# Kernel optimization log

Hardware: AMD Instinct MI355X
Metric: run time of the kernel (lower is better)

## Reference

```python
import jax, jax.numpy as jnp
import numpy as np

N_ITERS = 21
TEMPERATURE = 0.01


def setup_inputs() -> dict:
    key = jax.random.key(0)
    input_tensor = jax.random.normal(key, (512, 256, 256), dtype=jnp.float32)
    return {"input_tensor": input_tensor}


def reference(input_tensor) -> jnp.ndarray:
    # log_alpha: [B, n, n]
    n = input_tensor.shape[1]
    log_alpha = input_tensor.reshape(-1, n, n) / TEMPERATURE

    def body(i, la):
        # row normalization (sum over dim 2), then column normalization (sum over dim 1)
        la = la - jax.nn.logsumexp(la, axis=2, keepdims=True)
        la = la - jax.nn.logsumexp(la, axis=1, keepdims=True)
        return la

    log_alpha = jax.lax.fori_loop(0, N_ITERS, body, log_alpha)
    return jnp.exp(log_alpha)
```

## Files before the change

### kernel.cpp

```cpp
#include <hip/hip_runtime.h>

typedef __attribute__((ext_vector_type(2))) float f32x2;

#define N 256
#define BLK 1024
#define N_ITERS 21

template <int CTRL>
__device__ __forceinline__ float dppmov(float v) {
  return __int_as_float(__builtin_amdgcn_update_dpp(
      0, __float_as_int(v), CTRL, 0xF, 0xF, true));
}
__device__ __forceinline__ float swz_xor16(float v) {
  return __int_as_float(
      __builtin_amdgcn_ds_swizzle(__float_as_int(v), 0x401F));
}
__device__ __forceinline__ float rsum32(float v) {
  v += dppmov<0x121>(v);
  v += dppmov<0x122>(v);
  v += dppmov<0x124>(v);
  v += dppmov<0x128>(v);
  v += swz_xor16(v);
  return v;
}
__device__ __forceinline__ float rmax32(float v) {
  v = fmaxf(v, dppmov<0x121>(v));
  v = fmaxf(v, dppmov<0x122>(v));
  v = fmaxf(v, dppmov<0x124>(v));
  v = fmaxf(v, dppmov<0x128>(v));
  v = fmaxf(v, swz_xor16(v));
  return v;
}
__device__ __forceinline__ f32x2 pkmax(f32x2 a, f32x2 b) {
  f32x2 r;
  r.x = fmaxf(a.x, b.x);
  r.y = fmaxf(a.y, b.y);
  return r;
}

__global__ __launch_bounds__(BLK, 2)
void sinkhorn_kernel(const float* __restrict__ x, float* __restrict__ out) {
  __shared__ float lds_part[32 * N];
  __shared__ float lds_v[N];

  const int tid = threadIdx.x;
  const int cg = tid & 31;
  const int rg = tid >> 5;
  const int r0 = rg * 8;
  const long mat = blockIdx.x;
  const float SCALE = 144.2695040888963407f;

  const int cr = tid >> 2;
  const int q = tid & 3;
  const int cg_r = cr & 31;
  const int k_r = cr >> 5;
  const int red_base = k_r * 32;
  const int vslot = k_r * 32 + cg_r;

  const float4* __restrict__ src4 =
      reinterpret_cast<const float4*>(x + mat * (long)(N * N));
  f32x2 p[8][4];
  #pragma unroll
  for (int r = 0; r < 8; ++r) {
    float4 a = src4[(r0 + r) * 64 + cg * 2];
    float4 b = src4[(r0 + r) * 64 + cg * 2 + 1];
    f32x2 t;
    t.x = a.x; t.y = a.y; p[r][0] = t * SCALE;
    t.x = a.z; t.y = a.w; p[r][1] = t * SCALE;
    t.x = b.x; t.y = b.y; p[r][2] = t * SCALE;
    t.x = b.z; t.y = b.w; p[r][3] = t * SCALE;
  }

  f32x2 Vr[4];

  #pragma unroll
  for (int r = 0; r < 8; ++r) {
    f32x2 m2 = pkmax(pkmax(p[r][0], p[r][1]), pkmax(p[r][2], p[r][3]));
    float m = rmax32(fmaxf(m2.x, m2.y));
    float s = 0.f;
    #pragma unroll
    for (int j = 0; j < 4; ++j) {
      s += __builtin_amdgcn_exp2f(p[r][j].x - m);
      s += __builtin_amdgcn_exp2f(p[r][j].y - m);
    }
    s = rsum32(s);
    float L = m + __builtin_amdgcn_logf(s);
    #pragma unroll
    for (int j = 0; j < 4; ++j) p[r][j] -= L;
  }
  {
    f32x2 cm[4];
    #pragma unroll
    for (int j = 0; j < 4; ++j) cm[j] = p[0][j];
    #pragma unroll
    for (int r = 1; r < 8; ++r)
      #pragma unroll
      for (int j = 0; j < 4; ++j) cm[j] = pkmax(cm[j], p[r][j]);
    const int wslot = (cg + rg) & 31;
    #pragma unroll
    for (int j = 0; j < 4; ++j) {
      lds_part[rg * N + (2 * j) * 32 + wslot] = cm[j].x;
      lds_part[rg * N + (2 * j + 1) * 32 + wslot] = cm[j].y;
    }
    __syncthreads();
    float M = -3.0e38f;
    #pragma unroll
    for (int jj = 0; jj < 8; ++jj) {
      int h = q * 8 + jj;
      M = fmaxf(M, lds_part[h * N + red_base + ((cg_r + h) & 31)]);
    }
    M = fmaxf(M, dppmov<0xB1>(M));
    M = fmaxf(M, dppmov<0x4E>(M));
    if (q == 0) lds_v[vslot] = M;
    __syncthreads();
    f32x2 Mk[4];
    #pragma unroll
    for (int j = 0; j < 4; ++j) {
      Mk[j].x = lds_v[(2 * j) * 32 + cg];
      Mk[j].y = lds_v[(2 * j + 1) * 32 + cg];
    }
    f32x2 ps[4];
    #pragma unroll
    for (int j = 0; j < 4; ++j) { ps[j].x = 0.f; ps[j].y = 0.f; }
    #pragma unroll
    for (int r = 0; r < 8; ++r) {
      #pragma unroll
      for (int j = 0; j < 4; ++j) {
        f32x2 v;
        v.x = __builtin_amdgcn_exp2f(p[r][j].x - Mk[j].x);
        v.y = __builtin_amdgcn_exp2f(p[r][j].y - Mk[j].y);
        p[r][j] = v;
        ps[j] += v;
      }
    }
    #pragma unroll
    for (int j = 0; j < 4; ++j) {
      lds_part[rg * N + (2 * j) * 32 + wslot] = ps[j].x;
      lds_part[rg * N + (2 * j + 1) * 32 + wslot] = ps[j].y;
    }
    __syncthreads();
    float S = 0.f;
    #pragma unroll
    for (int jj = 0; jj < 8; ++jj) {
      int h = q * 8 + jj;
      S += lds_part[h * N + red_base + ((cg_r + h) & 31)];
    }
    S += dppmov<0xB1>(S);
    S += dppmov<0x4E>(S);
    if (q == 0) lds_v[vslot] = __builtin_amdgcn_rcpf(S);
    __syncthreads();
    #pragma unroll
    for (int j = 0; j < 4; ++j) {
      Vr[j].x = lds_v[(2 * j) * 32 + cg];
      Vr[j].y = lds_v[(2 * j + 1) * 32 + cg];
    }
  }

  for (int it = 1; it < N_ITERS; ++it) {
    f32x2 ps[4];
    #pragma unroll
    for (int j = 0; j < 4; ++j) { ps[j].x = 0.f; ps[j].y = 0.f; }
    #pragma unroll
    for (int r = 0; r < 8; ++r) {
      p[r][0] *= Vr[0]; p[r][1] *= Vr[1];
      p[r][2] *= Vr[2]; p[r][3] *= Vr[3];
      f32x2 t = (p[r][0] + p[r][1]) + (p[r][2] + p[r][3]);
      float g = __builtin_amdgcn_rcpf(rsum32(t.x + t.y));
      p[r][0] *= g; p[r][1] *= g; p[r][2] *= g; p[r][3] *= g;
      ps[0] += p[r][0]; ps[1] += p[r][1];
      ps[2] += p[r][2]; ps[3] += p[r][3];
    }
    const int wslot = (cg + rg) & 31;
    #pragma unroll
    for (int j = 0; j < 4; ++j) {
      lds_part[rg * N + (2 * j) * 32 + wslot] = ps[j].x;
      lds_part[rg * N + (2 * j + 1) * 32 + wslot] = ps[j].y;
    }
    __syncthreads();
    float S = 0.f;
    #pragma unroll
    for (int jj = 0; jj < 8; ++jj) {
      int h = q * 8 + jj;
      S += lds_part[h * N + red_base + ((cg_r + h) & 31)];
    }
    S += dppmov<0xB1>(S);
    S += dppmov<0x4E>(S);
    if (q == 0) lds_v[vslot] = __builtin_amdgcn_rcpf(S);
    __syncthreads();
    #pragma unroll
    for (int j = 0; j < 4; ++j) {
      Vr[j].x = lds_v[(2 * j) * 32 + cg];
      Vr[j].y = lds_v[(2 * j + 1) * 32 + cg];
    }
  }

  float4* __restrict__ dst4 =
      reinterpret_cast<float4*>(out + mat * (long)(N * N));
  #pragma unroll
  for (int r = 0; r < 8; ++r) {
    f32x2 a = p[r][0] * Vr[0];
    f32x2 b = p[r][1] * Vr[1];
    f32x2 c = p[r][2] * Vr[2];
    f32x2 d = p[r][3] * Vr[3];
    dst4[(r0 + r) * 64 + cg * 2] = make_float4(a.x, a.y, b.x, b.y);
    dst4[(r0 + r) * 64 + cg * 2 + 1] = make_float4(c.x, c.y, d.x, d.y);
  }
}

extern "C" void kernel_launch(void* const* d_in, const int* in_sizes, int n_in,
                              void* d_out, int out_size, void* d_ws, size_t ws_size,
                              hipStream_t stream) {
  const float* x = (const float*)d_in[0];
  float* out = (float*)d_out;
  int B = in_sizes[0] / (N * N);
  hipLaunchKernelGGL(sinkhorn_kernel, dim3(B), dim3(BLK), 0, stream, x, out);
}
```

Baseline: 135.8 us.

## Replace LDS tree reductions with triple-buffered LDS atomics and permlane swaps

Column sums and the initial column max are now accumulated with LDS atomicAdd/atomicMin into small triple-rotated buffers rather than written as partials and re-reduced. This cuts each Sinkhorn iteration to one barrier instead of two. The max relies on uint ordering of non-positive floats, which holds because values are log-normalized. Cross-half exchanges use permlane16/32_swap where available instead of ds_swizzle. The cost is 16-way atomic contention per LDS slot.

```diff
diff --git a/kernel.cpp b/kernel.cpp
--- a/kernel.cpp
+++ b/kernel.cpp
@@ -1,35 +1,91 @@
 #include <hip/hip_runtime.h>
 
 typedef __attribute__((ext_vector_type(2))) float f32x2;
+typedef unsigned int uintv2 __attribute__((ext_vector_type(2)));
 
 #define N 256
 #define BLK 1024
-#define N_ITERS 21
+#define SLOTS 290
 
 template <int CTRL>
 __device__ __forceinline__ float dppmov(float v) {
   return __int_as_float(__builtin_amdgcn_update_dpp(
       0, __float_as_int(v), CTRL, 0xF, 0xF, true));
 }
-__device__ __forceinline__ float swz_xor16(float v) {
-  return __int_as_float(
-      __builtin_amdgcn_ds_swizzle(__float_as_int(v), 0x401F));
-}
+
+#if __has_builtin(__builtin_amdgcn_permlane16_swap)
+__device__ __forceinline__ float xor16_add(float x) {
+  uintv2 r = __builtin_amdgcn_permlane16_swap(__float_as_uint(x),
+                                              __float_as_uint(x), false, false);
+  return __uint_as_float(r.x) + __uint_as_float(r.y);
+}
+__device__ __forceinline__ float xor16_max(float x) {
+  uintv2 r = __builtin_amdgcn_permlane16_swap(__float_as_uint(x),
+                                              __float_as_uint(x), false, false);
+  return fmaxf(__uint_as_float(r.x), __uint_as_float(r.y));
+}
+#else
+__device__ __forceinline__ float xor16_add(float x) {
+  return x + __int_as_float(
+                 __builtin_amdgcn_ds_swizzle(__float_as_int(x), 0x401F));
+}
+__device__ __forceinline__ float xor16_max(float x) {
+  return fmaxf(x, __int_as_float(__builtin_amdgcn_ds_swizzle(
+                      __float_as_int(x), 0x401F)));
+}
+#endif
+
+#if __has_builtin(__builtin_amdgcn_permlane32_swap)
+__device__ __forceinline__ void pair32(float x, float& lo, float& hi) {
+  uintv2 r = __builtin_amdgcn_permlane32_swap(__float_as_uint(x),
+                                              __float_as_uint(x), false, false);
+  lo = __uint_as_float(r.x);
+  hi = __uint_as_float(r.y);
+}
+__device__ __forceinline__ float swap32_add(float a, float b) {
+  uintv2 r = __builtin_amdgcn_permlane32_swap(__float_as_uint(a),
+                                              __float_as_uint(b), false, false);
+  return __uint_as_float(r.x) + __uint_as_float(r.y);
+}
+__device__ __forceinline__ float swap32_max(float a, float b) {
+  uintv2 r = __builtin_amdgcn_permlane32_swap(__float_as_uint(a),
+                                              __float_as_uint(b), false, false);
+  return fmaxf(__uint_as_float(r.x), __uint_as_float(r.y));
+}
+#else
+__device__ __forceinline__ void pair32(float x, float& lo, float& hi) {
+  float o = __shfl_xor(x, 32);
+  bool up = (threadIdx.x & 32) != 0;
+  lo = up ? o : x;
+  hi = up ? x : o;
+}
+__device__ __forceinline__ float swap32_add(float a, float b) {
+  bool up = (threadIdx.x & 32) != 0;
+  float mine = up ? b : a;
+  float send = up ? a : b;
+  return mine + __shfl_xor(send, 32);
+}
+__device__ __forceinline__ float swap32_max(float a, float b) {
+  bool up = (threadIdx.x & 32) != 0;
+  float mine = up ? b : a;
+  float send = up ? a : b;
+  return fmaxf(mine, __shfl_xor(send, 32));
+}
+#endif
+
 __device__ __forceinline__ float rsum32(float v) {
   v += dppmov<0x121>(v);
   v += dppmov<0x122>(v);
   v += dppmov<0x124>(v);
   v += dppmov<0x128>(v);
-  v += swz_xor16(v);
-  return v;
+  return xor16_add(v);
 }
 __device__ __forceinline__ float rmax32(float v) {
   v = fmaxf(v, dppmov<0x121>(v));
   v = fmaxf(v, dppmov<0x122>(v));
   v = fmaxf(v, dppmov<0x124>(v));
   v = fmaxf(v, dppmov<0x128>(v));
-  v = fmaxf(v, swz_xor16(v));
-  return v;
+  return xor16_max(v);
 }
 __device__ __forceinline__ f32x2 pkmax(f32x2 a, f32x2 b) {
   f32x2 r;
@@ -38,24 +94,59 @@
   return r;
 }
 
+__device__ __forceinline__ void prob_iter(f32x2 (&p)[8][4], f32x2 (&Vr)[4],
+                                          float* WR, float* ZR, int slot,
+                                          int hi) {
+  f32x2 ps[4];
+  ps[0] = ps[1] = ps[2] = ps[3] = (f32x2){0.f, 0.f};
+  #pragma unroll
+  for (int r = 0; r < 8; ++r) {
+    p[r][0] *= Vr[0]; p[r][1] *= Vr[1];
+    p[r][2] *= Vr[2]; p[r][3] *= Vr[3];
+    f32x2 t2 = (p[r][0] + p[r][1]) + (p[r][2] + p[r][3]);
+    float g = __builtin_amdgcn_rcpf(rsum32(t2.x + t2.y));
+    p[r][0] *= g; p[r][1] *= g; p[r][2] *= g; p[r][3] *= g;
+    ps[0] += p[r][0]; ps[1] += p[r][1];
+    ps[2] += p[r][2]; ps[3] += p[r][3];
+  }
+  const float psf[8] = {ps[0].x, ps[0].y, ps[1].x, ps[1].y,
+                        ps[2].x, ps[2].y, ps[3].x, ps[3].y};
+  #pragma unroll
+  for (int j = 0; j < 4; ++j)
+    atomicAdd(&WR[slot + j], swap32_add(psf[j], psf[j + 4]));
+  #pragma unroll
+  for (int j = 0; j < 4; ++j) ZR[slot + j] = 0.f;
+  __syncthreads();
+  float vf[8];
+  #pragma unroll
+  for (int j = 0; j < 4; ++j) {
+    float s = __builtin_amdgcn_rcpf(WR[slot + j]);
+    pair32(s, vf[j], vf[j + 4]);
+  }
+  Vr[0] = (f32x2){vf[0], vf[1]};
+  Vr[1] = (f32x2){vf[2], vf[3]};
+  Vr[2] = (f32x2){vf[4], vf[5]};
+  Vr[3] = (f32x2){vf[6], vf[7]};
+}
+
 __global__ __launch_bounds__(BLK, 2)
 void sinkhorn_kernel(const float* __restrict__ x, float* __restrict__ out) {
-  __shared__ float lds_part[32 * N];
-  __shared__ float lds_v[N];
+  __shared__ float S0[SLOTS], S1[SLOTS], S2[SLOTS];
 
   const int tid = threadIdx.x;
   const int cg = tid & 31;
   const int rg = tid >> 5;
   const int r0 = rg * 8;
+  const int hi = rg & 1;
+  const int slot = 9 * cg + hi * 4;
   const long mat = blockIdx.x;
   const float SCALE = 144.2695040888963407f;
 
-  const int cr = tid >> 2;
-  const int q = tid & 3;
-  const int cg_r = cr & 31;
-  const int k_r = cr >> 5;
-  const int red_base = k_r * 32;
-  const int vslot = k_r * 32 + cg_r;
+  if (tid < SLOTS) {
+    S0[tid] = 0.f;
+    S1[tid] = 0.f;
+    reinterpret_cast<unsigned*>(S2)[tid] = 0xFFFFFFFFu;
+  }
 
   const float4* __restrict__ src4 =
       reinterpret_cast<const float4*>(x + mat * (long)(N * N));
@@ -71,8 +162,6 @@
     t.x = b.z; t.y = b.w; p[r][3] = t * SCALE;
   }
 
-  f32x2 Vr[4];
-
   #pragma unroll
   for (int r = 0; r < 8; ++r) {
     f32x2 m2 = pkmax(pkmax(p[r][0], p[r][1]), pkmax(p[r][2], p[r][3]));
@@ -88,111 +177,73 @@
     #pragma unroll
     for (int j = 0; j < 4; ++j) p[r][j] -= L;
   }
+  __syncthreads();
+
   {
     f32x2 cm[4];
     #pragma unroll
     for (int j = 0; j < 4; ++j) cm[j] = p[0][j];
     #pragma unroll
-    for (int r = 1; r < 8; ++r)
+    for (int r = 1; r < 8; ++r) {
       #pragma unroll
       for (int j = 0; j < 4; ++j) cm[j] = pkmax(cm[j], p[r][j]);
-    const int wslot = (cg + rg) & 31;
+    }
+    const float cmf[8] = {cm[0].x, cm[0].y, cm[1].x, cm[1].y,
+                          cm[2].x, cm[2].y, cm[3].x, cm[3].y};
+    unsigned* S2u = reinterpret_cast<unsigned*>(S2);
+    #pragma unroll
+    for (int j = 0; j < 4; ++j)
+      atomicMin(&S2u[slot + j],
+                __float_as_uint(swap32_max(cmf[j], cmf[j + 4])));
+    __syncthreads();
+    float Mf[8];
     #pragma unroll
     for (int j = 0; j < 4; ++j) {
-      lds_part[rg * N + (2 * j) * 32 + wslot] = cm[j].x;
-      lds_part[rg * N + (2 * j + 1) * 32 + wslot] = cm[j].y;
-    }
-    __syncthreads();
-    float M = -3.0e38f;
-    #pragma unroll
-    for (int jj = 0; jj < 8; ++jj) {
-      int h = q * 8 + jj;
-      M = fmaxf(M, lds_part[h * N + red_base + ((cg_r + h) & 31)]);
-    }
-    M = fmaxf(M, dppmov<0xB1>(M));
-    M = fmaxf(M, dppmov<0x4E>(M));
-    if (q == 0) lds_v[vslot] = M;
-    __syncthreads();
-    f32x2 Mk[4];
-    #pragma unroll
-    for (int j = 0; j < 4; ++j) {
-      Mk[j].x = lds_v[(2 * j) * 32 + cg];
-      Mk[j].y = lds_v[(2 * j + 1) * 32 + cg];
+      float xx = __uint_as_float(S2u[slot + j]);
+      pair32(xx, Mf[j], Mf[j + 4]);
     }
     f32x2 ps[4];
-    #pragma unroll
-    for (int j = 0; j < 4; ++j) { ps[j].x = 0.f; ps[j].y = 0.f; }
+    ps[0] = ps[1] = ps[2] = ps[3] = (f32x2){0.f, 0.f};
     #pragma unroll
     for (int r = 0; r < 8; ++r) {
       #pragma unroll
-      for (int j = 0; j < 4; ++j) {
+      for (int k = 0; k < 4; ++k) {
         f32x2 v;
-        v.x = __builtin_amdgcn_exp2f(p[r][j].x - Mk[j].x);
-        v.y = __builtin_amdgcn_exp2f(p[r][j].y - Mk[j].y);
-        p[r][j] = v;
-        ps[j] += v;
+        v.x = __builtin_amdgcn_exp2f(p[r][k].x - Mf[2 * k]);
+        v.y = __builtin_amdgcn_exp2f(p[r][k].y - Mf[2 * k + 1]);
+        p[r][k] = v;
+        ps[k] += v;
       }
     }
+    const float psf[8] = {ps[0].x, ps[0].y, ps[1].x, ps[1].y,
+                          ps[2].x, ps[2].y, ps[3].x, ps[3].y};
+    #pragma unroll
+    for (int j = 0; j < 4; ++j)
+      atomicAdd(&S0[slot + j], swap32_add(psf[j], psf[j + 4]));
+    __syncthreads();
+  }
+  f32x2 Vr[4];
+  {
+    float vf[8];
     #pragma unroll
     for (int j = 0; j < 4; ++j) {
-      lds_part[rg * N + (2 * j) * 32 + wslot] = ps[j].x;
-      lds_part[rg * N + (2 * j + 1) * 32 + wslot] = ps[j].y;
-    }
-    __syncthreads();
-    float S = 0.f;
-    #pragma unroll
-    for (int jj = 0; jj < 8; ++jj) {
-      int h = q * 8 + jj;
-      S += lds_part[h * N + red_base + ((cg_r + h) & 31)];
-    }
-    S += dppmov<0xB1>(S);
-    S += dppmov<0x4E>(S);
-    if (q == 0) lds_v[vslot] = __builtin_amdgcn_rcpf(S);
-    __syncthreads();
-    #pragma unroll
-    for (int j = 0; j < 4; ++j) {
-      Vr[j].x = lds_v[(2 * j) * 32 + cg];
-      Vr[j].y = lds_v[(2 * j + 1) * 32 + cg];
-    }
-  }
-
-  for (int it = 1; it < N_ITERS; ++it) {
-    f32x2 ps[4];
-    #pragma unroll
-    for (int j = 0; j < 4; ++j) { ps[j].x = 0.f; ps[j].y = 0.f; }
-    #pragma unroll
-    for (int r = 0; r < 8; ++r) {
-      p[r][0] *= Vr[0]; p[r][1] *= Vr[1];
-      p[r][2] *= Vr[2]; p[r][3] *= Vr[3];
-      f32x2 t = (p[r][0] + p[r][1]) + (p[r][2] + p[r][3]);
-      float g = __builtin_amdgcn_rcpf(rsum32(t.x + t.y));
-      p[r][0] *= g; p[r][1] *= g; p[r][2] *= g; p[r][3] *= g;
-      ps[0] += p[r][0]; ps[1] += p[r][1];
-      ps[2] += p[r][2]; ps[3] += p[r][3];
-    }
-    const int wslot = (cg + rg) & 31;
-    #pragma unroll
-    for (int j = 0; j < 4; ++j) {
-      lds_part[rg * N + (2 * j) * 32 + wslot] = ps[j].x;
-      lds_part[rg * N + (2 * j + 1) * 32 + wslot] = ps[j].y;
-    }
-    __syncthreads();
-    float S = 0.f;
-    #pragma unroll
-    for (int jj = 0; jj < 8; ++jj) {
-      int h = q * 8 + jj;
-      S += lds_part[h * N + red_base + ((cg_r + h) & 31)];
-    }
-    S += dppmov<0xB1>(S);
-    S += dppmov<0x4E>(S);
-    if (q == 0) lds_v[vslot] = __builtin_amdgcn_rcpf(S);
-    __syncthreads();
-    #pragma unroll
-    for (int j = 0; j < 4; ++j) {
-      Vr[j].x = lds_v[(2 * j) * 32 + cg];
-      Vr[j].y = lds_v[(2 * j + 1) * 32 + cg];
-    }
-  }
+      float s = __builtin_amdgcn_rcpf(S0[slot + j]);
+      pair32(s, vf[j], vf[j + 4]);
+    }
+    Vr[0] = (f32x2){vf[0], vf[1]};
+    Vr[1] = (f32x2){vf[2], vf[3]};
+    Vr[2] = (f32x2){vf[4], vf[5]};
+    Vr[3] = (f32x2){vf[6], vf[7]};
+  }
+
+  #pragma unroll 1
+  for (int u = 0; u < 6; ++u) {
+    prob_iter(p, Vr, S1, S2, slot, hi);
+    prob_iter(p, Vr, S2, S0, slot, hi);
+    prob_iter(p, Vr, S0, S1, slot, hi);
+  }
+  prob_iter(p, Vr, S1, S2, slot, hi);
+  prob_iter(p, Vr, S2, S0, slot, hi);
 
   float4* __restrict__ dst4 =
       reinterpret_cast<float4*>(out + mat * (long)(N * N));
```

Result: slower. 300.9 us (+121.6%).
